# Kernel optimization log

Hardware: AMD Instinct MI355X
Metric: run time of the kernel (lower is better)

The kernel has to match this reference:

```python
import jax, jax.numpy as jnp
import numpy as np

EPS = 1e-4  # softmax_kernel eps

def softmax_kernel(data, projection, is_query):
    # data: [b,h,n,d], projection: [m,d]
    d = data.shape[-1]
    m = projection.shape[0]
    data_normalizer = d ** -0.25
    ratio = m ** -0.5
    data_dash = jnp.einsum('bhnd,md->bhnm', data_normalizer * data, projection)
    diag_data = (jnp.sum(data ** 2, axis=-1) * 0.5 * data_normalizer ** 2)[..., None]  # [b,h,n,1]
    if is_query:
        stab = jnp.max(data_dash, axis=-1, keepdims=True)
    else:
        stab = jnp.max(data_dash)
    return ratio * (jnp.exp(data_dash - diag_data - stab) + EPS)

def linear_attention(q, k, v):
    # q,k: [b,h,n,m]; v: [b,h,n,e]
    k_cumsum = jnp.sum(k, axis=-2)                                  # [b,h,m]
    D_inv = 1.0 / jnp.einsum('bhnm,bhm->bhn', q, k_cumsum)          # [b,h,n]
    context = jnp.einsum('bhnm,bhne->bhme', k, v)                   # [b,h,m,e]
    return jnp.einsum('bhme,bhnm,bhn->bhne', context, q, D_inv)     # [b,h,n,e]

def setup_inputs() -> dict:
    key = jax.random.key(0)
    kq, kk, kv, kp = jax.random.split(key, 4)
    B, H, N, D = 4, 8, 4096, 64
    M = 266  # int(64 * ln(64))
    q = jax.random.normal(kq, (B, H, N, D), dtype=jnp.float32)
    k = jax.random.normal(kk, (B, H, N, D), dtype=jnp.float32)
    v = jax.random.normal(kv, (B, H, N, D), dtype=jnp.float32)
    # Gaussian random-feature projection (stand-in for orthogonal blocks; same math path)
    projection = jax.random.normal(kp, (M, D), dtype=jnp.float32)
    return {"q": q, "k": k, "v": v, "projection": projection}

def reference(q, k, v, projection):
    q_prime = softmax_kernel(q, projection, is_query=True)
    k_prime = softmax_kernel(k, projection, is_query=False)
    return linear_attention(q_prime, k_prime, v)
```

## Files before the change

### kernel.cpp

```cpp
#include <hip/hip_runtime.h>
#include <math.h>

#define BHX 32
#define NN 4096
#define DD 64
#define MM 266
#define MP 272
#define NORMZ 0.35355339059327379f
#define RATIO 0.06131393394849658f
#define EPSV 1e-4f
#define NEG_INF (-3.4e38f)
#define LSTR 72
#define GSTR 320

typedef __attribute__((ext_vector_type(8))) short bfrag;
typedef __attribute__((ext_vector_type(4))) float f32x4;

#define MFMA(a, b, c) __builtin_amdgcn_mfma_f32_16x16x32_bf16((a), (b), (c), 0, 0, 0)

__device__ inline ushort bf16rne(float x) {
    union { float f; unsigned u; } c; c.f = x;
    unsigned r = c.u + 0x7FFFu + ((c.u >> 16) & 1u);
    return (ushort)(r >> 16);
}
__device__ inline float bf2f(ushort h) {
    union { unsigned u; float f; } c; c.u = ((unsigned)h) << 16;
    return c.f;
}
__device__ inline void splitf(float x, ushort& h, ushort& l) {
    h = bf16rne(x);
    l = bf16rne(x - bf2f(h));
}

__global__ void proj_split(const float* __restrict__ proj,
                           ushort* __restrict__ pH, ushort* __restrict__ pL)
{
    int i = (blockIdx.x * 256 + threadIdx.x) * 4;
    int m = i >> 6;
    float4 x = (m < MM) ? *(const float4*)(proj + i) : make_float4(0.f, 0.f, 0.f, 0.f);
    ushort h0, l0, h1, l1, h2, l2, h3, l3;
    splitf(x.x, h0, l0); splitf(x.y, h1, l1); splitf(x.z, h2, l2); splitf(x.w, h3, l3);
    *(ushort4*)(pH + i) = make_ushort4(h0, h1, h2, h3);
    *(ushort4*)(pL + i) = make_ushort4(l0, l1, l2, l3);
}

__global__ void vsum_kernel(const float* __restrict__ v, float* __restrict__ vsum)
{
    __shared__ float red[4][64];
    const int t = threadIdx.x, hd = blockIdx.y, nc = blockIdx.x;
    const int e = t & 63, g = t >> 6;
    const float* vb = v + ((size_t)hd * NN + nc * 512) * DD;
    float s = 0.f;
    for (int j = 0; j < 128; ++j) s += vb[(j * 4 + g) * DD + e];
    red[g][e] = s;
    __syncthreads();
    if (t < 64) atomicAdd(&vsum[hd * DD + t], red[0][t] + red[1][t] + red[2][t] + red[3][t]);
}

__global__ void reduce_max_kernel(const float* __restrict__ partmax,
                                  float* __restrict__ stab, int n)
{
    __shared__ float sm[256];
    const int t = threadIdx.x;
    float mx = NEG_INF;
    for (int i = t; i < n; i += 256) mx = fmaxf(mx, partmax[i]);
    sm[t] = mx;
    __syncthreads();
    for (int s = 128; s > 0; s >>= 1) {
        if (t < s) sm[t] = fmaxf(sm[t], sm[t + s]);
        __syncthreads();
    }
    if (t == 0) *stab = sm[0];
}

__launch_bounds__(256, 2)
__global__ void kpass(const float* __restrict__ kin, const float* __restrict__ vin,
                      const ushort* __restrict__ pjH, const ushort* __restrict__ pjL,
                      float* __restrict__ ctxP, float* __restrict__ kcP,
                      float* __restrict__ pmax)
{
    __shared__ ushort dataH[64 * LSTR], dataLo[64 * LSTR];
    __shared__ ushort vTH[64 * LSTR], vTLo[64 * LSTR];
    __shared__ ushort r2H[64 * LSTR], r2Lo[64 * LSTR];
    __shared__ float diagS[64];
    __shared__ float kcS[MP];
    __shared__ float redS[4];

    const int t = threadIdx.x;
    const int w = t >> 6;
    const int lane = t & 63;
    const int l15 = lane & 15;
    const int q = lane >> 4;
    const int hd = blockIdx.y;
    const int nb = blockIdx.x;

    if (t < 256) kcS[t] = 0.f;
    if (t < 16) kcS[256 + t] = 0.f;

    const f32x4 zf = {0.f, 0.f, 0.f, 0.f};
    f32x4 cacc[4][4];
    f32x4 cacc4 = zf;
    #pragma unroll
    for (int c = 0; c < 4; ++c)
        #pragma unroll
        for (int e = 0; e < 4; ++e) cacc[c][e] = zf;
    float bmaxl = NEG_INF;

    #pragma unroll 1
    for (int st = 0; st < 4; ++st) {
        const int n0 = (nb << 8) + (st << 6);
        __syncthreads();

        const float* kb = kin + ((size_t)hd * NN + n0) * DD;
        #pragma unroll
        for (int j = 0; j < 4; ++j) {
            int i = (t + (j << 8)) << 2;
            int r = i >> 6, cc = i & 63;
            float4 x = *(const float4*)(kb + i);
            float x0 = x.x * NORMZ, x1 = x.y * NORMZ, x2 = x.z * NORMZ, x3 = x.w * NORMZ;
            ushort h0, l0, h1, l1, h2, l2, h3, l3;
            splitf(x0, h0, l0); splitf(x1, h1, l1); splitf(x2, h2, l2); splitf(x3, h3, l3);
            *(ushort4*)&dataH[r * LSTR + cc] = make_ushort4(h0, h1, h2, h3);
            *(ushort4*)&dataLo[r * LSTR + cc] = make_ushort4(l0, l1, l2, l3);
            float ss = x0 * x0 + x1 * x1 + x2 * x2 + x3 * x3;
            #pragma unroll
            for (int d = 1; d < 16; d <<= 1) ss += __shfl_xor(ss, d);
            if (l15 == 0) diagS[r] = 0.5f * ss;
        }
        const float* vb = vin + ((size_t)hd * NN + n0) * DD;
        #pragma unroll
        for (int j = 0; j < 4; ++j) {
            int i = (t + (j << 8)) << 2;
            int n = i >> 6, e = i & 63;
            float4 x = *(const float4*)(vb + i);
            ushort h, l;
            splitf(x.x, h, l); vTH[(e + 0) * LSTR + n] = h; vTLo[(e + 0) * LSTR + n] = l;
            splitf(x.y, h, l); vTH[(e + 1) * LSTR + n] = h; vTLo[(e + 1) * LSTR + n] = l;
            splitf(x.z, h, l); vTH[(e + 2) * LSTR + n] = h; vTLo[(e + 2) * LSTR + n] = l;
            splitf(x.w, h, l); vTH[(e + 3) * LSTR + n] = h; vTLo[(e + 3) * LSTR + n] = l;
        }
        __syncthreads();

        bfrag aH[2], aL[2];
        {
            const int row = (w << 4) + l15;
            aH[0] = *(const bfrag*)&dataH[row * LSTR + (q << 3)];
            aH[1] = *(const bfrag*)&dataH[row * LSTR + 32 + (q << 3)];
            aL[0] = *(const bfrag*)&dataLo[row * LSTR + (q << 3)];
            aL[1] = *(const bfrag*)&dataLo[row * LSTR + 32 + (q << 3)];
        }

        #pragma unroll
        for (int c = 0; c < 5; ++c) {
            const int mtiles = (c < 4) ? 4 : 1;
            const int m0 = c << 6;
            {
                const int tot = mtiles << 7;
                for (int idx = t; idx < tot; idx += 256) {
                    int i = idx << 3; int r = i >> 6, cc = i & 63;
                    *(uint4*)&r2H[r * LSTR + cc] = *(const uint4*)(pjH + ((m0 + r) << 6) + cc);
                    *(uint4*)&r2Lo[r * LSTR + cc] = *(const uint4*)(pjL + ((m0 + r) << 6) + cc);
                }
            }
            __syncthreads();

            f32x4 dd4[4];
            #pragma unroll
            for (int mt = 0; mt < 4; ++mt) {
                if (mt >= mtiles) break;
                const int mrow = (mt << 4) + l15;
                bfrag bH0 = *(const bfrag*)&r2H[mrow * LSTR + (q << 3)];
                bfrag bH1 = *(const bfrag*)&r2H[mrow * LSTR + 32 + (q << 3)];
                bfrag bL0 = *(const bfrag*)&r2Lo[mrow * LSTR + (q << 3)];
                bfrag bL1 = *(const bfrag*)&r2Lo[mrow * LSTR + 32 + (q << 3)];
                f32x4 a = zf;
                a = MFMA(aH[0], bL0, a);
                a = MFMA(aH[1], bL1, a);
                a = MFMA(aL[0], bH0, a);
                a = MFMA(aL[1], bH1, a);
                a = MFMA(aH[0], bH0, a);
                a = MFMA(aH[1], bH1, a);
                dd4[mt] = a;
            }
            #pragma unroll
            for (int mt = 0; mt < 4; ++mt) {
                if (mt >= mtiles) break;
                const int mg = m0 + (mt << 4) + l15;
                const bool valid = (mg < MM);
                ushort uh[4], ul[4];
                float csum = 0.f;
                #pragma unroll
                for (int reg = 0; reg < 4; ++reg) {
                    float dv = dd4[mt][reg];
                    float u = 0.f;
                    if (valid) {
                        bmaxl = fmaxf(bmaxl, dv);
                        u = __expf(dv - diagS[(w << 4) + (q << 2) + reg]);
                    }
                    csum += u;
                    splitf(u, uh[reg], ul[reg]);
                }
                *(ushort4*)&dataH[((mt << 4) + l15) * LSTR + (w << 4) + (q << 2)] =
                    make_ushort4(uh[0], uh[1], uh[2], uh[3]);
                *(ushort4*)&dataLo[((mt << 4) + l15) * LSTR + (w << 4) + (q << 2)] =
                    make_ushort4(ul[0], ul[1], ul[2], ul[3]);
                csum += __shfl_xor(csum, 16);
                csum += __shfl_xor(csum, 32);
                if (q == 0) atomicAdd(&kcS[mg], csum);
            }
            __syncthreads();

            if (c < 4) {
                const int mrow = (w << 4) + l15;
                bfrag uH0 = *(const bfrag*)&dataH[mrow * LSTR + (q << 3)];
                bfrag uH1 = *(const bfrag*)&dataH[mrow * LSTR + 32 + (q << 3)];
                bfrag uL0 = *(const bfrag*)&dataLo[mrow * LSTR + (q << 3)];
                bfrag uL1 = *(const bfrag*)&dataLo[mrow * LSTR + 32 + (q << 3)];
                #pragma unroll
                for (int et = 0; et < 4; ++et) {
                    const int erow = (et << 4) + l15;
                    bfrag vH0 = *(const bfrag*)&vTH[erow * LSTR + (q << 3)];
                    bfrag vH1 = *(const bfrag*)&vTH[erow * LSTR + 32 + (q << 3)];
                    bfrag vL0 = *(const bfrag*)&vTLo[erow * LSTR + (q << 3)];
                    bfrag vL1 = *(const bfrag*)&vTLo[erow * LSTR + 32 + (q << 3)];
                    f32x4 a = cacc[c][et];
                    a = MFMA(uH0, vL0, a);
                    a = MFMA(uH1, vL1, a);
                    a = MFMA(uL0, vH0, a);
                    a = MFMA(uL1, vH1, a);
                    a = MFMA(uH0, vH0, a);
                    a = MFMA(uH1, vH1, a);
                    cacc[c][et] = a;
                }
            } else {
                const int mrow = l15;
                bfrag uH0 = *(const bfrag*)&dataH[mrow * LSTR + (q << 3)];
                bfrag uH1 = *(const bfrag*)&dataH[mrow * LSTR + 32 + (q << 3)];
                bfrag uL0 = *(const bfrag*)&dataLo[mrow * LSTR + (q << 3)];
                bfrag uL1 = *(const bfrag*)&dataLo[mrow * LSTR + 32 + (q << 3)];
                const int erow = (w << 4) + l15;
                bfrag vH0 = *(const bfrag*)&vTH[erow * LSTR + (q << 3)];
                bfrag vH1 = *(const bfrag*)&vTH[erow * LSTR + 32 + (q << 3)];
                bfrag vL0 = *(const bfrag*)&vTLo[erow * LSTR + (q << 3)];
                bfrag vL1 = *(const bfrag*)&vTLo[erow * LSTR + 32 + (q << 3)];
                f32x4 a = cacc4;
                a = MFMA(uH0, vL0, a);
                a = MFMA(uH1, vL1, a);
                a = MFMA(uL0, vH0, a);
                a = MFMA(uL1, vH1, a);
                a = MFMA(uH0, vH0, a);
                a = MFMA(uH1, vH1, a);
                cacc4 = a;
            }
        }
    }

    __syncthreads();
    {
        float bm = bmaxl;
        #pragma unroll
        for (int d = 1; d < 64; d <<= 1) bm = fmaxf(bm, __shfl_xor(bm, d));
        if (lane == 0) redS[w] = bm;
    }
    __syncthreads();
    if (t == 0) pmax[hd * 16 + nb] = fmaxf(fmaxf(redS[0], redS[1]), fmaxf(redS[2], redS[3]));
    for (int m = t; m < MP; m += 256) kcP[(size_t)(hd * 16 + nb) * MP + m] = kcS[m];
    float* cp = ctxP + (size_t)(hd * 16 + nb) * MP * DD;
    #pragma unroll
    for (int c = 0; c < 4; ++c) {
        const int mbase = (c << 6) + (w << 4) + (q << 2);
        #pragma unroll
        for (int et = 0; et < 4; ++et)
            #pragma unroll
            for (int reg = 0; reg < 4; ++reg)
                cp[(mbase + reg) * DD + (et << 4) + l15] = cacc[c][et][reg];
    }
    #pragma unroll
    for (int reg = 0; reg < 4; ++reg)
        cp[(256 + (q << 2) + reg) * DD + (w << 4) + l15] = cacc4[reg];
}

__global__ void ctx_reduce(const float* __restrict__ ctxP, const float* __restrict__ kcP,
                           const float* __restrict__ vsum, const float* __restrict__ stabp,
                           ushort* __restrict__ gH, ushort* __restrict__ gL)
{
    __shared__ ushort hiT[64][20], loT[64][20];
    const int t = threadIdx.x, mt = blockIdx.x, hd = blockIdx.y;
    const float Asc = RATIO * __expf(-*stabp);
    const float REPS = RATIO * EPSV;
    const int e = t & 63, mq = t >> 6;
    const float vs = vsum[hd * DD + e];
    #pragma unroll
    for (int i = 0; i < 4; ++i) {
        const int ml = mq * 4 + i;
        const int m = mt * 16 + ml;
        float s = 0.f;
        for (int nbk = 0; nbk < 16; ++nbk)
            s += ctxP[((size_t)(hd * 16 + nbk) * MP + m) * DD + e];
        float val = Asc * s + REPS * vs;
        ushort h, l; splitf(val, h, l);
        hiT[e][ml] = h; loT[e][ml] = l;
    }
    __syncthreads();
    {
        const int i = t * 4, e2 = i >> 4, cc = i & 15;
        ushort4 hv = make_ushort4(hiT[e2][cc], hiT[e2][cc + 1], hiT[e2][cc + 2], hiT[e2][cc + 3]);
        ushort4 lv = make_ushort4(loT[e2][cc], loT[e2][cc + 1], loT[e2][cc + 2], loT[e2][cc + 3]);
        *(ushort4*)(gH + ((size_t)hd * 80 + e2) * GSTR + mt * 16 + cc) = hv;
        *(ushort4*)(gL + ((size_t)hd * 80 + e2) * GSTR + mt * 16 + cc) = lv;
    }
    if (t < 16) {
        const int m = mt * 16 + t;
        float s = 0.f;
        for (int nbk = 0; nbk < 16; ++nbk) s += kcP[(size_t)(hd * 16 + nbk) * MP + m];
        float val = Asc * s + ((m < MM) ? REPS * (float)NN : 0.f);
        ushort h, l; splitf(val, h, l);
        gH[((size_t)hd * 80 + 64) * GSTR + m] = h;
        gL[((size_t)hd * 80 + 64) * GSTR + m] = l;
    }
}

__launch_bounds__(256, 2)
__global__ void qpass(const float* __restrict__ qin,
                      const ushort* __restrict__ pjH, const ushort* __restrict__ pjL,
                      const ushort* __restrict__ gH, const ushort* __restrict__ gL,
                      float* __restrict__ outp)
{
    __shared__ ushort dataH[64 * LSTR], dataLo[64 * LSTR];
    __shared__ ushort r2H[64 * LSTR], r2Lo[64 * LSTR];
    __shared__ ushort cbH[80 * LSTR], cbLo[80 * LSTR];
    __shared__ float diagS[64];

    const int t = threadIdx.x;
    const int w = t >> 6;
    const int lane = t & 63;
    const int l15 = lane & 15;
    const int q = lane >> 4;
    const int hd = blockIdx.y;
    const int n0 = blockIdx.x << 6;

    const float* qb = qin + ((size_t)hd * NN + n0) * DD;
    #pragma unroll
    for (int j = 0; j < 4; ++j) {
        int i = (t + (j << 8)) << 2;
        int r = i >> 6, cc = i & 63;
        float4 x = *(const float4*)(qb + i);
        float x0 = x.x * NORMZ, x1 = x.y * NORMZ, x2 = x.z * NORMZ, x3 = x.w * NORMZ;
        ushort h0, l0, h1, l1, h2, l2, h3, l3;
        splitf(x0, h0, l0); splitf(x1, h1, l1); splitf(x2, h2, l2); splitf(x3, h3, l3);
        *(ushort4*)&dataH[r * LSTR + cc] = make_ushort4(h0, h1, h2, h3);
        *(ushort4*)&dataLo[r * LSTR + cc] = make_ushort4(l0, l1, l2, l3);
        float ss = x0 * x0 + x1 * x1 + x2 * x2 + x3 * x3;
        #pragma unroll
        for (int d = 1; d < 16; d <<= 1) ss += __shfl_xor(ss, d);
        if (l15 == 0) diagS[r] = 0.5f * ss;
    }
    __syncthreads();

    bfrag aH[2], aL[2];
    {
        const int row = (w << 4) + l15;
        aH[0] = *(const bfrag*)&dataH[row * LSTR + (q << 3)];
        aH[1] = *(const bfrag*)&dataH[row * LSTR + 32 + (q << 3)];
        aL[0] = *(const bfrag*)&dataLo[row * LSTR + (q << 3)];
        aL[1] = *(const bfrag*)&dataLo[row * LSTR + 32 + (q << 3)];
    }

    const f32x4 zf = {0.f, 0.f, 0.f, 0.f};
    f32x4 ddq[17];

    #pragma unroll
    for (int c = 0; c < 5; ++c) {
        const int mtiles = (c < 4) ? 4 : 1;
        const int m0 = c << 6;
        __syncthreads();
        {
            const int tot = mtiles << 7;
            for (int idx = t; idx < tot; idx += 256) {
                int i = idx << 3; int r = i >> 6, cc = i & 63;
                *(uint4*)&r2H[r * LSTR + cc] = *(const uint4*)(pjH + ((m0 + r) << 6) + cc);
                *(uint4*)&r2Lo[r * LSTR + cc] = *(const uint4*)(pjL + ((m0 + r) << 6) + cc);
            }
        }
        __syncthreads();
        #pragma unroll
        for (int mt = 0; mt < 4; ++mt) {
            if (mt >= mtiles) break;
            const int mrow = (mt << 4) + l15;
            bfrag bH0 = *(const bfrag*)&r2H[mrow * LSTR + (q << 3)];
            bfrag bH1 = *(const bfrag*)&r2H[mrow * LSTR + 32 + (q << 3)];
            bfrag bL0 = *(const bfrag*)&r2Lo[mrow * LSTR + (q << 3)];
            bfrag bL1 = *(const bfrag*)&r2Lo[mrow * LSTR + 32 + (q << 3)];
            f32x4 a = zf;
            a = MFMA(aH[0], bL0, a);
            a = MFMA(aH[1], bL1, a);
            a = MFMA(aL[0], bH0, a);
            a = MFMA(aL[1], bH1, a);
            a = MFMA(aH[0], bH0, a);
            a = MFMA(aH[1], bH1, a);
            ddq[c * 4 + mt] = a;
        }
    }

    float rmax[4];
    #pragma unroll
    for (int reg = 0; reg < 4; ++reg) {
        float mx = NEG_INF;
        #pragma unroll
        for (int ti = 0; ti < 17; ++ti) {
            bool valid = (ti < 16) || (l15 < 10);
            if (valid) mx = fmaxf(mx, ddq[ti][reg]);
        }
        #pragma unroll
        for (int d = 1; d < 16; d <<= 1) mx = fmaxf(mx, __shfl_xor(mx, d));
        rmax[reg] = mx;
    }
    #pragma unroll
    for (int ti = 0; ti < 17; ++ti) {
        #pragma unroll
        for (int reg = 0; reg < 4; ++reg) {
            bool valid = (ti < 16) || (l15 < 10);
            float e = 0.f;
            if (valid)
                e = RATIO * (__expf(ddq[ti][reg] - diagS[(w << 4) + (q << 2) + reg] - rmax[reg]) + EPSV);
            ddq[ti][reg] = e;
        }
    }

    f32x4 oacc[5];
    #pragma unroll
    for (int et = 0; et < 5; ++et) oacc[et] = zf;

    #pragma unroll
    for (int c = 0; c < 5; ++c) {
        const int mtiles = (c < 4) ? 4 : 1;
        __syncthreads();
        {
            for (int idx = t; idx < 640; idx += 256) {
                int i = idx << 3; int e = i >> 6, mm = i & 63;
                *(uint4*)&cbH[e * LSTR + mm] =
                    *(const uint4*)(gH + ((size_t)hd * 80 + e) * GSTR + (c << 6) + mm);
                *(uint4*)&cbLo[e * LSTR + mm] =
                    *(const uint4*)(gL + ((size_t)hd * 80 + e) * GSTR + (c << 6) + mm);
            }
        }
        #pragma unroll
        for (int mt = 0; mt < 4; ++mt) {
            if (mt >= mtiles) break;
            const int ml = (mt << 4) + l15;
            #pragma unroll
            for (int reg = 0; reg < 4; ++reg) {
                ushort h, l; splitf(ddq[c * 4 + mt][reg], h, l);
                r2H[((w << 4) + (q << 2) + reg) * LSTR + ml] = h;
                r2Lo[((w << 4) + (q << 2) + reg) * LSTR + ml] = l;
            }
        }
        if (c == 4) {
            const int rown = (w << 4) + l15;
            *(ushort4*)&r2H[rown * LSTR + 16 + (q << 2)] = make_ushort4(0, 0, 0, 0);
            *(ushort4*)&r2Lo[rown * LSTR + 16 + (q << 2)] = make_ushort4(0, 0, 0, 0);
        }
        __syncthreads();
        const int arow = (w << 4) + l15;
        bfrag pH0 = *(const bfrag*)&r2H[arow * LSTR + (q << 3)];
        bfrag pL0 = *(const bfrag*)&r2Lo[arow * LSTR + (q << 3)];
        bfrag pH1, pL1;
        if (c < 4) {
            pH1 = *(const bfrag*)&r2H[arow * LSTR + 32 + (q << 3)];
            pL1 = *(const bfrag*)&r2Lo[arow * LSTR + 32 + (q << 3)];
        }
        #pragma unroll
        for (int et = 0; et < 5; ++et) {
            const int erow = (et << 4) + l15;
            bfrag cH0 = *(const bfrag*)&cbH[erow * LSTR + (q << 3)];
            bfrag cL0 = *(const bfrag*)&cbLo[erow * LSTR + (q << 3)];
            f32x4 a = oacc[et];
            a = MFMA(pH0, cL0, a);
            a = MFMA(pL0, cH0, a);
            a = MFMA(pH0, cH0, a);
            if (c < 4) {
                bfrag cH1 = *(const bfrag*)&cbH[erow * LSTR + 32 + (q << 3)];
                bfrag cL1 = *(const bfrag*)&cbLo[erow * LSTR + 32 + (q << 3)];
                a = MFMA(pH1, cL1, a);
                a = MFMA(pL1, cH1, a);
                a = MFMA(pH1, cH1, a);
            }
            oacc[et] = a;
        }
    }

    float dinv[4];
    #pragma unroll
    for (int reg = 0; reg < 4; ++reg) {
        float den = __shfl(oacc[4][reg], lane & 48);
        dinv[reg] = 1.f / den;
    }
    float* ob = outp + ((size_t)hd * NN + n0) * DD;
    #pragma unroll
    for (int et = 0; et < 4; ++et)
        #pragma unroll
        for (int reg = 0; reg < 4; ++reg)
            ob[((w << 4) + (q << 2) + reg) * DD + (et << 4) + l15] = oacc[et][reg] * dinv[reg];
}

extern "C" void kernel_launch(void* const* d_in, const int* in_sizes, int n_in,
                              void* d_out, int out_size, void* d_ws, size_t ws_size,
                              hipStream_t stream)
{
    const float* q = (const float*)d_in[0];
    const float* k = (const float*)d_in[1];
    const float* v = (const float*)d_in[2];
    const float* proj = (const float*)d_in[3];
    float* out = (float*)d_out;
    char* ws = (char*)d_ws;

    ushort* gH = (ushort*)(ws);
    ushort* gL = (ushort*)(ws + 1638400);
    float* vsm = (float*)(ws + 3276800);
    ushort* pH = (ushort*)(ws + 3284992);
    ushort* pL = (ushort*)(ws + 3319808);
    float* ctxP = (float*)(ws + 3354624);
    float* kcP = (float*)(ws + 39006208);
    float* pmax = (float*)(ws + 39563264);
    float* stab = (float*)(ws + 39565312);

    hipMemsetAsync(ws, 0, 3284992, stream);

    proj_split<<<dim3(17), 256, 0, stream>>>(proj, pH, pL);
    vsum_kernel<<<dim3(8, 32), 256, 0, stream>>>(v, vsm);
    kpass<<<dim3(16, 32), 256, 0, stream>>>(k, v, pH, pL, ctxP, kcP, pmax);
    reduce_max_kernel<<<1, 256, 0, stream>>>(pmax, stab, 512);
    ctx_reduce<<<dim3(17, 32), 256, 0, stream>>>(ctxP, kcP, vsm, stab, gH, gL);
    qpass<<<dim3(64, 32), 256, 0, stream>>>(q, pH, pL, gH, gL, out);
}
```

Before: 278.2 us.

## Fuse vsum and max reduction into kpass/ctx_reduce, retile kpass for occupancy

```diff
diff --git a/kernel.cpp b/kernel.cpp
--- a/kernel.cpp
+++ b/kernel.cpp
@@ -44,44 +44,15 @@
     *(ushort4*)(pL + i) = make_ushort4(l0, l1, l2, l3);
 }
 
-__global__ void vsum_kernel(const float* __restrict__ v, float* __restrict__ vsum)
-{
-    __shared__ float red[4][64];
-    const int t = threadIdx.x, hd = blockIdx.y, nc = blockIdx.x;
-    const int e = t & 63, g = t >> 6;
-    const float* vb = v + ((size_t)hd * NN + nc * 512) * DD;
-    float s = 0.f;
-    for (int j = 0; j < 128; ++j) s += vb[(j * 4 + g) * DD + e];
-    red[g][e] = s;
-    __syncthreads();
-    if (t < 64) atomicAdd(&vsum[hd * DD + t], red[0][t] + red[1][t] + red[2][t] + red[3][t]);
-}
-
-__global__ void reduce_max_kernel(const float* __restrict__ partmax,
-                                  float* __restrict__ stab, int n)
-{
-    __shared__ float sm[256];
-    const int t = threadIdx.x;
-    float mx = NEG_INF;
-    for (int i = t; i < n; i += 256) mx = fmaxf(mx, partmax[i]);
-    sm[t] = mx;
-    __syncthreads();
-    for (int s = 128; s > 0; s >>= 1) {
-        if (t < s) sm[t] = fmaxf(sm[t], sm[t + s]);
-        __syncthreads();
-    }
-    if (t == 0) *stab = sm[0];
-}
-
-__launch_bounds__(256, 2)
+__launch_bounds__(256, 3)
 __global__ void kpass(const float* __restrict__ kin, const float* __restrict__ vin,
                       const ushort* __restrict__ pjH, const ushort* __restrict__ pjL,
                       float* __restrict__ ctxP, float* __restrict__ kcP,
-                      float* __restrict__ pmax)
+                      float* __restrict__ pmax, float* __restrict__ vsumg)
 {
-    __shared__ ushort dataH[64 * LSTR], dataLo[64 * LSTR];
-    __shared__ ushort vTH[64 * LSTR], vTLo[64 * LSTR];
-    __shared__ ushort r2H[64 * LSTR], r2Lo[64 * LSTR];
+    __shared__ __align__(16) ushort uH[64 * LSTR], uLo[64 * LSTR];
+    __shared__ __align__(16) ushort vH[64 * LSTR], vLo[64 * LSTR];
+    __shared__ __align__(16) ushort rpH[32 * LSTR], rpL[32 * LSTR];
     __shared__ float diagS[64];
     __shared__ float kcS[MP];
     __shared__ float redS[4];
@@ -91,24 +62,26 @@
     const int lane = t & 63;
     const int l15 = lane & 15;
     const int q = lane >> 4;
-    const int hd = blockIdx.y;
-    const int nb = blockIdx.x;
+    const int hd = blockIdx.y, nb = blockIdx.x;
+    const int npart = gridDim.x;
+    const int nsub = (NN / npart) >> 6;
 
     if (t < 256) kcS[t] = 0.f;
     if (t < 16) kcS[256 + t] = 0.f;
 
     const f32x4 zf = {0.f, 0.f, 0.f, 0.f};
-    f32x4 cacc[4][4];
-    f32x4 cacc4 = zf;
-    #pragma unroll
-    for (int c = 0; c < 4; ++c)
-        #pragma unroll
-        for (int e = 0; e < 4; ++e) cacc[c][e] = zf;
+    f32x4 cacc[8][2];
+    f32x4 cacc8 = zf;
+    #pragma unroll
+    for (int c = 0; c < 8; ++c)
+        #pragma unroll
+        for (int je = 0; je < 2; ++je) cacc[c][je] = zf;
     float bmaxl = NEG_INF;
+    float vsAcc = 0.f;
 
     #pragma unroll 1
-    for (int st = 0; st < 4; ++st) {
-        const int n0 = (nb << 8) + (st << 6);
+    for (int st = 0; st < nsub; ++st) {
+        const int n0 = nb * (nsub << 6) + (st << 6);
         __syncthreads();
 
         const float* kb = kin + ((size_t)hd * NN + n0) * DD;
@@ -120,59 +93,65 @@
             float x0 = x.x * NORMZ, x1 = x.y * NORMZ, x2 = x.z * NORMZ, x3 = x.w * NORMZ;
             ushort h0, l0, h1, l1, h2, l2, h3, l3;
             splitf(x0, h0, l0); splitf(x1, h1, l1); splitf(x2, h2, l2); splitf(x3, h3, l3);
-            *(ushort4*)&dataH[r * LSTR + cc] = make_ushort4(h0, h1, h2, h3);
-            *(ushort4*)&dataLo[r * LSTR + cc] = make_ushort4(l0, l1, l2, l3);
+            *(ushort4*)&uH[r * LSTR + cc] = make_ushort4(h0, h1, h2, h3);
+            *(ushort4*)&uLo[r * LSTR + cc] = make_ushort4(l0, l1, l2, l3);
             float ss = x0 * x0 + x1 * x1 + x2 * x2 + x3 * x3;
             #pragma unroll
             for (int d = 1; d < 16; d <<= 1) ss += __shfl_xor(ss, d);
             if (l15 == 0) diagS[r] = 0.5f * ss;
         }
         const float* vb = vin + ((size_t)hd * NN + n0) * DD;
-        #pragma unroll
-        for (int j = 0; j < 4; ++j) {
-            int i = (t + (j << 8)) << 2;
-            int n = i >> 6, e = i & 63;
-            float4 x = *(const float4*)(vb + i);
-            ushort h, l;
-            splitf(x.x, h, l); vTH[(e + 0) * LSTR + n] = h; vTLo[(e + 0) * LSTR + n] = l;
-            splitf(x.y, h, l); vTH[(e + 1) * LSTR + n] = h; vTLo[(e + 1) * LSTR + n] = l;
-            splitf(x.z, h, l); vTH[(e + 2) * LSTR + n] = h; vTLo[(e + 2) * LSTR + n] = l;
-            splitf(x.w, h, l); vTH[(e + 3) * LSTR + n] = h; vTLo[(e + 3) * LSTR + n] = l;
+        {
+            const int ve = lane;
+            #pragma unroll
+            for (int jj = 0; jj < 4; ++jj) {
+                const int nq = w + (jj << 2);
+                float x0 = vb[((nq << 2) + 0) * DD + ve];
+                float x1 = vb[((nq << 2) + 1) * DD + ve];
+                float x2 = vb[((nq << 2) + 2) * DD + ve];
+                float x3 = vb[((nq << 2) + 3) * DD + ve];
+                vsAcc += x0 + x1 + x2 + x3;
+                ushort h0, l0, h1, l1, h2, l2, h3, l3;
+                splitf(x0, h0, l0); splitf(x1, h1, l1);
+                splitf(x2, h2, l2); splitf(x3, h3, l3);
+                *(ushort4*)&vH[ve * LSTR + (nq << 2)] = make_ushort4(h0, h1, h2, h3);
+                *(ushort4*)&vLo[ve * LSTR + (nq << 2)] = make_ushort4(l0, l1, l2, l3);
+            }
         }
         __syncthreads();
 
         bfrag aH[2], aL[2];
         {
             const int row = (w << 4) + l15;
-            aH[0] = *(const bfrag*)&dataH[row * LSTR + (q << 3)];
-            aH[1] = *(const bfrag*)&dataH[row * LSTR + 32 + (q << 3)];
-            aL[0] = *(const bfrag*)&dataLo[row * LSTR + (q << 3)];
-            aL[1] = *(const bfrag*)&dataLo[row * LSTR + 32 + (q << 3)];
-        }
-
-        #pragma unroll
-        for (int c = 0; c < 5; ++c) {
-            const int mtiles = (c < 4) ? 4 : 1;
-            const int m0 = c << 6;
+            aH[0] = *(const bfrag*)&uH[row * LSTR + (q << 3)];
+            aH[1] = *(const bfrag*)&uH[row * LSTR + 32 + (q << 3)];
+            aL[0] = *(const bfrag*)&uLo[row * LSTR + (q << 3)];
+            aL[1] = *(const bfrag*)&uLo[row * LSTR + 32 + (q << 3)];
+        }
+
+        #pragma unroll
+        for (int c = 0; c < 9; ++c) {
+            const int mtiles = (c < 8) ? 2 : 1;
+            const int m0 = c << 5;
             {
-                const int tot = mtiles << 7;
-                for (int idx = t; idx < tot; idx += 256) {
+                const int tot8 = mtiles << 7;
+                for (int idx = t; idx < tot8; idx += 256) {
                     int i = idx << 3; int r = i >> 6, cc = i & 63;
-                    *(uint4*)&r2H[r * LSTR + cc] = *(const uint4*)(pjH + ((m0 + r) << 6) + cc);
-                    *(uint4*)&r2Lo[r * LSTR + cc] = *(const uint4*)(pjL + ((m0 + r) << 6) + cc);
+                    *(uint4*)&rpH[r * LSTR + cc] = *(const uint4*)(pjH + ((m0 + r) << 6) + cc);
+                    *(uint4*)&rpL[r * LSTR + cc] = *(const uint4*)(pjL + ((m0 + r) << 6) + cc);
                 }
             }
             __syncthreads();
 
-            f32x4 dd4[4];
-            #pragma unroll
-            for (int mt = 0; mt < 4; ++mt) {
+            f32x4 dd4[2];
+            #pragma unroll
+            for (int mt = 0; mt < 2; ++mt) {
                 if (mt >= mtiles) break;
                 const int mrow = (mt << 4) + l15;
-                bfrag bH0 = *(const bfrag*)&r2H[mrow * LSTR + (q << 3)];
-                bfrag bH1 = *(const bfrag*)&r2H[mrow * LSTR + 32 + (q << 3)];
-                bfrag bL0 = *(const bfrag*)&r2Lo[mrow * LSTR + (q << 3)];
-                bfrag bL1 = *(const bfrag*)&r2Lo[mrow * LSTR + 32 + (q << 3)];
+                bfrag bH0 = *(const bfrag*)&rpH[mrow * LSTR + (q << 3)];
+                bfrag bH1 = *(const bfrag*)&rpH[mrow * LSTR + 32 + (q << 3)];
+                bfrag bL0 = *(const bfrag*)&rpL[mrow * LSTR + (q << 3)];
+                bfrag bL1 = *(const bfrag*)&rpL[mrow * LSTR + 32 + (q << 3)];
                 f32x4 a = zf;
                 a = MFMA(aH[0], bL0, a);
                 a = MFMA(aH[1], bL1, a);
@@ -183,7 +162,7 @@
                 dd4[mt] = a;
             }
             #pragma unroll
-            for (int mt = 0; mt < 4; ++mt) {
+            for (int mt = 0; mt < 2; ++mt) {
                 if (mt >= mtiles) break;
                 const int mg = m0 + (mt << 4) + l15;
                 const bool valid = (mg < MM);
@@ -200,9 +179,9 @@
                     csum += u;
                     splitf(u, uh[reg], ul[reg]);
                 }
-                *(ushort4*)&dataH[((mt << 4) + l15) * LSTR + (w << 4) + (q << 2)] =
+                *(ushort4*)&uH[((mt << 4) + l15) * LSTR + (w << 4) + (q << 2)] =
                     make_ushort4(uh[0], uh[1], uh[2], uh[3]);
-                *(ushort4*)&dataLo[((mt << 4) + l15) * LSTR + (w << 4) + (q << 2)] =
+                *(ushort4*)&uLo[((mt << 4) + l15) * LSTR + (w << 4) + (q << 2)] =
                     make_ushort4(ul[0], ul[1], ul[2], ul[3]);
                 csum += __shfl_xor(csum, 16);
                 csum += __shfl_xor(csum, 32);
@@ -210,52 +189,55 @@
             }
             __syncthreads();
 
-            if (c < 4) {
-                const int mrow = (w << 4) + l15;
-                bfrag uH0 = *(const bfrag*)&dataH[mrow * LSTR + (q << 3)];
-                bfrag uH1 = *(const bfrag*)&dataH[mrow * LSTR + 32 + (q << 3)];
-                bfrag uL0 = *(const bfrag*)&dataLo[mrow * LSTR + (q << 3)];
-                bfrag uL1 = *(const bfrag*)&dataLo[mrow * LSTR + 32 + (q << 3)];
+            if (c < 8) {
+                const int tw = w & 1, eh0 = (w >> 1) << 1;
+                const int urow = (tw << 4) + l15;
+                bfrag uH0 = *(const bfrag*)&uH[urow * LSTR + (q << 3)];
+                bfrag uH1 = *(const bfrag*)&uH[urow * LSTR + 32 + (q << 3)];
+                bfrag uL0 = *(const bfrag*)&uLo[urow * LSTR + (q << 3)];
+                bfrag uL1 = *(const bfrag*)&uLo[urow * LSTR + 32 + (q << 3)];
                 #pragma unroll
-                for (int et = 0; et < 4; ++et) {
-                    const int erow = (et << 4) + l15;
-                    bfrag vH0 = *(const bfrag*)&vTH[erow * LSTR + (q << 3)];
-                    bfrag vH1 = *(const bfrag*)&vTH[erow * LSTR + 32 + (q << 3)];
-                    bfrag vL0 = *(const bfrag*)&vTLo[erow * LSTR + (q << 3)];
-                    bfrag vL1 = *(const bfrag*)&vTLo[erow * LSTR + 32 + (q << 3)];
-                    f32x4 a = cacc[c][et];
+                for (int je = 0; je < 2; ++je) {
+                    const int erow = ((eh0 + je) << 4) + l15;
+                    bfrag vH0 = *(const bfrag*)&vH[erow * LSTR + (q << 3)];
+                    bfrag vH1 = *(const bfrag*)&vH[erow * LSTR + 32 + (q << 3)];
+                    bfrag vL0 = *(const bfrag*)&vLo[erow * LSTR + (q << 3)];
+                    bfrag vL1 = *(const bfrag*)&vLo[erow * LSTR + 32 + (q << 3)];
+                    f32x4 a = cacc[c][je];
                     a = MFMA(uH0, vL0, a);
                     a = MFMA(uH1, vL1, a);
                     a = MFMA(uL0, vH0, a);
                     a = MFMA(uL1, vH1, a);
                     a = MFMA(uH0, vH0, a);
                     a = MFMA(uH1, vH1, a);
-                    cacc[c][et] = a;
+                    cacc[c][je] = a;
                 }
             } else {
-                const int mrow = l15;
-                bfrag uH0 = *(const bfrag*)&dataH[mrow * LSTR + (q << 3)];
-                bfrag uH1 = *(const bfrag*)&dataH[mrow * LSTR + 32 + (q << 3)];
-                bfrag uL0 = *(const bfrag*)&dataLo[mrow * LSTR + (q << 3)];
-                bfrag uL1 = *(const bfrag*)&dataLo[mrow * LSTR + 32 + (q << 3)];
+                const int urow = l15;
+                bfrag uH0 = *(const bfrag*)&uH[urow * LSTR + (q << 3)];
+                bfrag uH1 = *(const bfrag*)&uH[urow * LSTR + 32 + (q << 3)];
+                bfrag uL0 = *(const bfrag*)&uLo[urow * LSTR + (q << 3)];
+                bfrag uL1 = *(const bfrag*)&uLo[urow * LSTR + 32 + (q << 3)];
                 const int erow = (w << 4) + l15;
-                bfrag vH0 = *(const bfrag*)&vTH[erow * LSTR + (q << 3)];
-                bfrag vH1 = *(const bfrag*)&vTH[erow * LSTR + 32 + (q << 3)];
-                bfrag vL0 = *(const bfrag*)&vTLo[erow * LSTR + (q << 3)];
-                bfrag vL1 = *(const bfrag*)&vTLo[erow * LSTR + 32 + (q << 3)];
-                f32x4 a = cacc4;
+                bfrag vH0 = *(const bfrag*)&vH[erow * LSTR + (q << 3)];
+                bfrag vH1 = *(const bfrag*)&vH[erow * LSTR + 32 + (q << 3)];
+                bfrag vL0 = *(const bfrag*)&vLo[erow * LSTR + (q << 3)];
+                bfrag vL1 = *(const bfrag*)&vLo[erow * LSTR + 32 + (q << 3)];
+                f32x4 a = cacc8;
                 a = MFMA(uH0, vL0, a);
                 a = MFMA(uH1, vL1, a);
                 a = MFMA(uL0, vH0, a);
                 a = MFMA(uL1, vH1, a);
                 a = MFMA(uH0, vH0, a);
                 a = MFMA(uH1, vH1, a);
-                cacc4 = a;
+                cacc8 = a;
             }
         }
     }
 
     __syncthreads();
+    float* fsc = (float*)uH;
+    fsc[t] = vsAcc;
     {
         float bm = bmaxl;
         #pragma unroll
@@ -263,47 +245,64 @@
         if (lane == 0) redS[w] = bm;
     }
     __syncthreads();
-    if (t == 0) pmax[hd * 16 + nb] = fmaxf(fmaxf(redS[0], redS[1]), fmaxf(redS[2], redS[3]));
-    for (int m = t; m < MP; m += 256) kcP[(size_t)(hd * 16 + nb) * MP + m] = kcS[m];
-    float* cp = ctxP + (size_t)(hd * 16 + nb) * MP * DD;
-    #pragma unroll
-    for (int c = 0; c < 4; ++c) {
-        const int mbase = (c << 6) + (w << 4) + (q << 2);
-        #pragma unroll
-        for (int et = 0; et < 4; ++et)
+    if (t < 64) atomicAdd(&vsumg[hd * DD + t],
+                          fsc[t] + fsc[t + 64] + fsc[t + 128] + fsc[t + 192]);
+    if (t == 0) pmax[hd * npart + nb] =
+        fmaxf(fmaxf(redS[0], redS[1]), fmaxf(redS[2], redS[3]));
+    for (int m = t; m < MP; m += 256) kcP[(size_t)(hd * npart + nb) * MP + m] = kcS[m];
+
+    float* cp = ctxP + (size_t)(hd * npart + nb) * MP * DD;
+    #pragma unroll
+    for (int c = 0; c < 8; ++c) {
+        const int mbase = (c << 5) + ((w & 1) << 4) + (q << 2);
+        #pragma unroll
+        for (int je = 0; je < 2; ++je) {
+            const int ecol = ((((w >> 1) << 1) + je) << 4) + l15;
             #pragma unroll
             for (int reg = 0; reg < 4; ++reg)
-                cp[(mbase + reg) * DD + (et << 4) + l15] = cacc[c][et][reg];
+                cp[(mbase + reg) * DD + ecol] = cacc[c][je][reg];
+        }
     }
     #pragma unroll
     for (int reg = 0; reg < 4; ++reg)
-        cp[(256 + (q << 2) + reg) * DD + (w << 4) + l15] = cacc4[reg];
+        cp[(256 + (q << 2) + reg) * DD + (w << 4) + l15] = cacc8[reg];
 }
 
 __global__ void ctx_reduce(const float* __restrict__ ctxP, const float* __restrict__ kcP,
-                           const float* __restrict__ vsum, const float* __restrict__ stabp,
-                           ushort* __restrict__ gH, ushort* __restrict__ gL)
+                           const float* __restrict__ vsum, const float* __restrict__ pmax,
+                           ushort* __restrict__ gH, ushort* __restrict__ gL, int npart)
 {
+    __shared__ float smx[256];
     __shared__ ushort hiT[64][20], loT[64][20];
     const int t = threadIdx.x, mt = blockIdx.x, hd = blockIdx.y;
-    const float Asc = RATIO * __expf(-*stabp);
+
+    float mx = NEG_INF;
+    for (int i = t; i < npart * 32; i += 256) mx = fmaxf(mx, pmax[i]);
+    smx[t] = mx;
+    __syncthreads();
+    for (int s = 128; s > 0; s >>= 1) {
+        if (t < s) smx[t] = fmaxf(smx[t], smx[t + s]);
+        __syncthreads();
+    }
+    const float Asc = RATIO * __expf(-smx[0]);
     const float REPS = RATIO * EPSV;
+
     const int e = t & 63, mq = t >> 6;
     const float vs = vsum[hd * DD + e];
     #pragma unroll
     for (int i = 0; i < 4; ++i) {
-        const int ml = mq * 4 + i;
-        const int m = mt * 16 + ml;
+        const int ml = (mq << 2) + i;
+        const int m = (mt << 4) + ml;
         float s = 0.f;
-        for (int nbk = 0; nbk < 16; ++nbk)
-            s += ctxP[((size_t)(hd * 16 + nbk) * MP + m) * DD + e];
+        for (int nbk = 0; nbk < npart; ++nbk)
+            s += ctxP[((size_t)(hd * npart + nbk) * MP + m) * DD + e];
         float val = Asc * s + REPS * vs;
         ushort h, l; splitf(val, h, l);
         hiT[e][ml] = h; loT[e][ml] = l;
     }
     __syncthreads();
     {
-        const int i = t * 4, e2 = i >> 4, cc = i & 15;
+        const int i = t << 2, e2 = i >> 4, cc = i & 15;
         ushort4 hv = make_ushort4(hiT[e2][cc], hiT[e2][cc + 1], hiT[e2][cc + 2], hiT[e2][cc + 3]);
         ushort4 lv = make_ushort4(loT[e2][cc], loT[e2][cc + 1], loT[e2][cc + 2], loT[e2][cc + 3]);
         *(ushort4*)(gH + ((size_t)hd * 80 + e2) * GSTR + mt * 16 + cc) = hv;
@@ -312,7 +311,7 @@
     if (t < 16) {
         const int m = mt * 16 + t;
         float s = 0.f;
-        for (int nbk = 0; nbk < 16; ++nbk) s += kcP[(size_t)(hd * 16 + nbk) * MP + m];
+        for (int nbk = 0; nbk < npart; ++nbk) s += kcP[(size_t)(hd * npart + nbk) * MP + m];
         float val = Asc * s + ((m < MM) ? REPS * (float)NN : 0.f);
         ushort h, l; splitf(val, h, l);
         gH[((size_t)hd * 80 + 64) * GSTR + m] = h;
@@ -320,15 +319,14 @@
     }
 }
 
-__launch_bounds__(256, 2)
+__launch_bounds__(256, 3)
 __global__ void qpass(const float* __restrict__ qin,
                       const ushort* __restrict__ pjH, const ushort* __restrict__ pjL,
                       const ushort* __restrict__ gH, const ushort* __restrict__ gL,
                       float* __restrict__ outp)
 {
-    __shared__ ushort dataH[64 * LSTR], dataLo[64 * LSTR];
-    __shared__ ushort r2H[64 * LSTR], r2Lo[64 * LSTR];
-    __shared__ ushort cbH[80 * LSTR], cbLo[80 * LSTR];
+    __shared__ __align__(16) ushort r1H[64 * LSTR], r1L[64 * LSTR];
+    __shared__ __align__(16) ushort r2H[80 * LSTR], r2L[80 * LSTR];
     __shared__ float diagS[64];
 
     const int t = threadIdx.x;
@@ -348,8 +346,8 @@
         float x0 = x.x * NORMZ, x1 = x.y * NORMZ, x2 = x.z * NORMZ, x3 = x.w * NORMZ;
         ushort h0, l0, h1, l1, h2, l2, h3, l3;
         splitf(x0, h0, l0); splitf(x1, h1, l1); splitf(x2, h2, l2); splitf(x3, h3, l3);
-        *(ushort4*)&dataH[r * LSTR + cc] = make_ushort4(h0, h1, h2, h3);
-        *(ushort4*)&dataLo[r * LSTR + cc] = make_ushort4(l0, l1, l2, l3);
+        *(ushort4*)&r1H[r * LSTR + cc] = make_ushort4(h0, h1, h2, h3);
+        *(ushort4*)&r1L[r * LSTR + cc] = make_ushort4(l0, l1, l2, l3);
         float ss = x0 * x0 + x1 * x1 + x2 * x2 + x3 * x3;
         #pragma unroll
         for (int d = 1; d < 16; d <<= 1) ss += __shfl_xor(ss, d);
@@ -357,14 +355,15 @@
     }
     __syncthreads();
 
-    bfrag aH[2], aL[2];
+    bfrag dH0, dH1, dL0, dL1;
     {
         const int row = (w << 4) + l15;
-        aH[0] = *(const bfrag*)&dataH[row * LSTR + (q << 3)];
-        aH[1] = *(const bfrag*)&dataH[row * LSTR + 32 + (q << 3)];
-        aL[0] = *(const bfrag*)&dataLo[row * LSTR + (q << 3)];
-        aL[1] = *(const bfrag*)&dataLo[row * LSTR + 32 + (q << 3)];
-    }
+        dH0 = *(const bfrag*)&r1H[row * LSTR + (q << 3)];
+        dH1 = *(const bfrag*)&r1H[row * LSTR + 32 + (q << 3)];
+        dL0 = *(const bfrag*)&r1L[row * LSTR + (q << 3)];
+        dL1 = *(const bfrag*)&r1L[row * LSTR + 32 + (q << 3)];
+    }
+    const float dg = diagS[(w << 4) + l15];
 
     const f32x4 zf = {0.f, 0.f, 0.f, 0.f};
     f32x4 ddq[17];
@@ -375,11 +374,11 @@
         const int m0 = c << 6;
         __syncthreads();
         {
-            const int tot = mtiles << 7;
-            for (int idx = t; idx < tot; idx += 256) {
+            const int tot8 = mtiles << 7;
+            for (int idx = t; idx < tot8; idx += 256) {
                 int i = idx << 3; int r = i >> 6, cc = i & 63;
                 *(uint4*)&r2H[r * LSTR + cc] = *(const uint4*)(pjH + ((m0 + r) << 6) + cc);
-                *(uint4*)&r2Lo[r * LSTR + cc] = *(const uint4*)(pjL + ((m0 + r) << 6) + cc);
+                *(uint4*)&r2L[r * LSTR + cc] = *(const uint4*)(pjL + ((m0 + r) << 6) + cc);
             }
         }
         __syncthreads();
@@ -387,43 +386,41 @@
         for (int mt = 0; mt < 4; ++mt) {
             if (mt >= mtiles) break;
             const int mrow = (mt << 4) + l15;
-            bfrag bH0 = *(const bfrag*)&r2H[mrow * LSTR + (q << 3)];
-            bfrag bH1 = *(const bfrag*)&r2H[mrow * LSTR + 32 + (q << 3)];
-            bfrag bL0 = *(const bfrag*)&r2Lo[mrow * LSTR + (q << 3)];
-            bfrag bL1 = *(const bfrag*)&r2Lo[mrow * LSTR + 32 + (q << 3)];
+            bfrag pH0 = *(const bfrag*)&r2H[mrow * LSTR + (q << 3)];
+            bfrag pH1 = *(const bfrag*)&r2H[mrow * LSTR + 32 + (q << 3)];
+            bfrag pL0 = *(const bfrag*)&r2L[mrow * LSTR + (q << 3)];
+            bfrag pL1 = *(const bfrag*)&r2L[mrow * LSTR + 32 + (q << 3)];
             f32x4 a = zf;
-            a = MFMA(aH[0], bL0, a);
-            a = MFMA(aH[1], bL1, a);
-            a = MFMA(aL[0], bH0, a);
-            a = MFMA(aL[1], bH1, a);
-            a = MFMA(aH[0], bH0, a);
-            a = MFMA(aH[1], bH1, a);
-            ddq[c * 4 + mt] = a;
-        }
-    }
-
-    float rmax[4];
-    #pragma unroll
-    for (int reg = 0; reg < 4; ++reg) {
+            a = MFMA(pH0, dL0, a);
+            a = MFMA(pH1, dL1, a);
+            a = MFMA(pL0, dH0, a);
+            a = MFMA(pL1, dH1, a);
+            a = MFMA(pH0, dH0, a);
+            a = MFMA(pH1, dH1, a);
+            ddq[(c << 2) + mt] = a;
+        }
+    }
+
+    {
         float mx = NEG_INF;
         #pragma unroll
         for (int ti = 0; ti < 17; ++ti) {
-            bool valid = (ti < 16) || (l15 < 10);
-            if (valid) mx = fmaxf(mx, ddq[ti][reg]);
-        }
-        #pragma unroll
-        for (int d = 1; d < 16; d <<= 1) mx = fmaxf(mx, __shfl_xor(mx, d));
-        rmax[reg] = mx;
-    }
-    #pragma unroll
-    for (int ti = 0; ti < 17; ++ti) {
-        #pragma unroll
-        for (int reg = 0; reg < 4; ++reg) {
-            bool valid = (ti < 16) || (l15 < 10);
-            float e = 0.f;
-            if (valid)
-                e = RATIO * (__expf(ddq[ti][reg] - diagS[(w << 4) + (q << 2) + reg] - rmax[reg]) + EPSV);
-            ddq[ti][reg] = e;
+            #pragma unroll
+            for (int reg = 0; reg < 4; ++reg) {
+                bool valid = (ti < 16) || ((q << 2) + reg < 10);
+                if (valid) mx = fmaxf(mx, ddq[ti][reg]);
+            }
+        }
+        mx = fmaxf(mx, __shfl_xor(mx, 16));
+        mx = fmaxf(mx, __shfl_xor(mx, 32));
+        const float sub = dg + mx;
+        #pragma unroll
+        for (int ti = 0; ti < 17; ++ti) {
+            #pragma unroll
+            for (int reg = 0; reg < 4; ++reg) {
+                bool valid = (ti < 16) || ((q << 2) + reg < 10);
+                ddq[ti][reg] = valid ? (RATIO * (__expf(ddq[ti][reg] - sub) + EPSV)) : 0.f;
+            }
         }
     }
 
@@ -435,55 +432,53 @@
     for (int c = 0; c < 5; ++c) {
         const int mtiles = (c < 4) ? 4 : 1;
         __syncthreads();
-        {
-            for (int idx = t; idx < 640; idx += 256) {
-                int i = idx << 3; int e = i >> 6, mm = i & 63;
-                *(uint4*)&cbH[e * LSTR + mm] =
-                    *(const uint4*)(gH + ((size_t)hd * 80 + e) * GSTR + (c << 6) + mm);
-                *(uint4*)&cbLo[e * LSTR + mm] =
-                    *(const uint4*)(gL + ((size_t)hd * 80 + e) * GSTR + (c << 6) + mm);
-            }
+        for (int idx = t; idx < 640; idx += 256) {
+            int i = idx << 3; int e = i >> 6, mm = i & 63;
+            *(uint4*)&r2H[e * LSTR + mm] =
+                *(const uint4*)(gH + ((size_t)hd * 80 + e) * GSTR + (c << 6) + mm);
+            *(uint4*)&r2L[e * LSTR + mm] =
+                *(const uint4*)(gL + ((size_t)hd * 80 + e) * GSTR + (c << 6) + mm);
         }
         #pragma unroll
         for (int mt = 0; mt < 4; ++mt) {
             if (mt >= mtiles) break;
-            const int ml = (mt << 4) + l15;
-            #pragma unroll
-            for (int reg = 0; reg < 4; ++reg) {
-                ushort h, l; splitf(ddq[c * 4 + mt][reg], h, l);
-                r2H[((w << 4) + (q << 2) + reg) * LSTR + ml] = h;
-                r2Lo[((w << 4) + (q << 2) + reg) * LSTR + ml] = l;
-            }
+            ushort h0, l0, h1, l1, h2, l2, h3, l3;
+            f32x4 v = ddq[(c << 2) + mt];
+            splitf(v[0], h0, l0); splitf(v[1], h1, l1);
+            splitf(v[2], h2, l2); splitf(v[3], h3, l3);
+            *(ushort4*)&r1H[((w << 4) + l15) * LSTR + (mt << 4) + (q << 2)] =
+                make_ushort4(h0, h1, h2, h3);
+            *(ushort4*)&r1L[((w << 4) + l15) * LSTR + (mt << 4) + (q << 2)] =
+                make_ushort4(l0, l1, l2, l3);
         }
         if (c == 4) {
-            const int rown = (w << 4) + l15;
-            *(ushort4*)&r2H[rown * LSTR + 16 + (q << 2)] = make_ushort4(0, 0, 0, 0);
-            *(ushort4*)&r2Lo[rown * LSTR + 16 + (q << 2)] = make_ushort4(0, 0, 0, 0);
+            *(ushort4*)&r1H[((w << 4) + l15) * LSTR + 16 + (q << 2)] = make_ushort4(0, 0, 0, 0);
+            *(ushort4*)&r1L[((w << 4) + l15) * LSTR + 16 + (q << 2)] = make_ushort4(0, 0, 0, 0);
         }
         __syncthreads();
         const int arow = (w << 4) + l15;
-        bfrag pH0 = *(const bfrag*)&r2H[arow * LSTR + (q << 3)];
-        bfrag pL0 = *(const bfrag*)&r2Lo[arow * LSTR + (q << 3)];
-        bfrag pH1, pL1;
+        bfrag aH0 = *(const bfrag*)&r1H[arow * LSTR + (q << 3)];
+        bfrag aL0 = *(const bfrag*)&r1L[arow * LSTR + (q << 3)];
+        bfrag aH1, aL1;
         if (c < 4) {
-            pH1 = *(const bfrag*)&r2H[arow * LSTR + 32 + (q << 3)];
-            pL1 = *(const bfrag*)&r2Lo[arow * LSTR + 32 + (q << 3)];
+            aH1 = *(const bfrag*)&r1H[arow * LSTR + 32 + (q << 3)];
+            aL1 = *(const bfrag*)&r1L[arow * LSTR + 32 + (q << 3)];
         }
         #pragma unroll
         for (int et = 0; et < 5; ++et) {
             const int erow = (et << 4) + l15;
-            bfrag cH0 = *(const bfrag*)&cbH[erow * LSTR + (q << 3)];
-            bfrag cL0 = *(const bfrag*)&cbLo[erow * LSTR + (q << 3)];
+            bfrag cH0 = *(const bfrag*)&r2H[erow * LSTR + (q << 3)];
+            bfrag cL0 = *(const bfrag*)&r2L[erow * LSTR + (q << 3)];
             f32x4 a = oacc[et];
-            a = MFMA(pH0, cL0, a);
-            a = MFMA(pL0, cH0, a);
-            a = MFMA(pH0, cH0, a);
+            a = MFMA(aH0, cL0, a);
+            a = MFMA(aL0, cH0, a);
+            a = MFMA(aH0, cH0, a);
             if (c < 4) {
-                bfrag cH1 = *(const bfrag*)&cbH[erow * LSTR + 32 + (q << 3)];
-                bfrag cL1 = *(const bfrag*)&cbLo[erow * LSTR + 32 + (q << 3)];
-                a = MFMA(pH1, cL1, a);
-                a = MFMA(pL1, cH1, a);
-                a = MFMA(pH1, cH1, a);
+                bfrag cH1 = *(const bfrag*)&r2H[erow * LSTR + 32 + (q << 3)];
+                bfrag cL1 = *(const bfrag*)&r2L[erow * LSTR + 32 + (q << 3)];
+                a = MFMA(aH1, cL1, a);
+                a = MFMA(aL1, cH1, a);
+                a = MFMA(aH1, cH1, a);
             }
             oacc[et] = a;
         }
@@ -507,6 +502,7 @@
                               void* d_out, int out_size, void* d_ws, size_t ws_size,
                               hipStream_t stream)
 {
+    (void)in_sizes; (void)n_in; (void)out_size;
     const float* q = (const float*)d_in[0];
     const float* k = (const float*)d_in[1];
     const float* v = (const float*)d_in[2];
@@ -519,17 +515,20 @@
     float* vsm = (float*)(ws + 3276800);
     ushort* pH = (ushort*)(ws + 3284992);
     ushort* pL = (ushort*)(ws + 3319808);
-    float* ctxP = (float*)(ws + 3354624);
-    float* kcP = (float*)(ws + 39006208);
-    float* pmax = (float*)(ws + 39563264);
-    float* stab = (float*)(ws + 39565312);
+    const size_t base = 3354624;
+
+    const size_t need32 = base + (size_t)32 * 32 * MP * DD * 4
+                               + (size_t)32 * 32 * MP * 4 + (size_t)32 * 32 * 4;
+    const int npart = (ws_size >= need32) ? 32 : 16;
+
+    float* ctxP = (float*)(ws + base);
+    float* kcP  = ctxP + (size_t)npart * 32 * MP * DD;
+    float* pmax = kcP + (size_t)npart * 32 * MP;
 
     hipMemsetAsync(ws, 0, 3284992, stream);
 
     proj_split<<<dim3(17), 256, 0, stream>>>(proj, pH, pL);
-    vsum_kernel<<<dim3(8, 32), 256, 0, stream>>>(v, vsm);
-    kpass<<<dim3(16, 32), 256, 0, stream>>>(k, v, pH, pL, ctxP, kcP, pmax);
-    reduce_max_kernel<<<1, 256, 0, stream>>>(pmax, stab, 512);
-    ctx_reduce<<<dim3(17, 32), 256, 0, stream>>>(ctxP, kcP, vsm, stab, gH, gL);
+    kpass<<<dim3(npart, 32), 256, 0, stream>>>(k, v, pH, pL, ctxP, kcP, pmax, vsm);
+    ctx_reduce<<<dim3(17, 32), 256, 0, stream>>>(ctxP, kcP, vsm, pmax, gH, gL, npart);
     qpass<<<dim3(64, 32), 256, 0, stream>>>(q, pH, pL, gH, gL, out);
 }
```

After: 401.1 us. 44.2% more time.
